# Kernel optimization log

Hardware: AMD Instinct MI355X
Metric: run time of the kernel (lower is better)

Reference implementation:

```python
import jax, jax.numpy as jnp
import numpy as np

# Production GravNet config: 8 events x 4096 hits, K=40 neighbours, 4 spatial dims
B, V, K, S, P, F_IN, F_OUT = 8, 4096, 40, 4, 64, 64, 128
N = B * V
MAX_RADIUS_SQ = 1.0  # SelectKnn(max_radius=1.0)


def setup_inputs() -> dict:
    key = jax.random.key(0)
    ks = jax.random.split(key, 7)
    x = jax.random.normal(ks[0], (N, F_IN), jnp.float32)
    # Dense layer params (glorot-ish scaling)
    W_prop = jax.random.normal(ks[1], (F_IN, P), jnp.float32) / np.sqrt(F_IN)
    b_prop = jnp.zeros((P,), jnp.float32)
    W_sp = jax.random.normal(ks[2], (F_IN, S), jnp.float32) / np.sqrt(F_IN)
    b_sp = jnp.zeros((S,), jnp.float32)
    # output transform input dim = n_prop_total (2*P) + F_IN
    W_out = jax.random.normal(ks[3], (2 * P + F_IN, F_OUT), jnp.float32) / np.sqrt(2 * P + F_IN)
    b_out = jnp.zeros((F_OUT,), jnp.float32)
    row_splits = jnp.arange(B + 1, dtype=jnp.int32) * V  # equal-size ragged segments
    return dict(x=x, W_prop=W_prop, b_prop=b_prop, W_sp=W_sp, b_sp=b_sp,
                W_out=W_out, b_out=b_out, row_splits=row_splits)


def _knn_indices(coords):
    """Per-event brute-force KNN. coords: [N,S] -> global neighbour idx [N,K]."""
    c = coords.reshape(B, V, S)
    # pairwise squared distances within each event: [B,V,V]
    d = jnp.sum((c[:, :, None, :] - c[:, None, :, :]) ** 2, axis=-1)
    neg_d, idx = jax.lax.top_k(-d, K + 1)  # nearest first; col 0 is self (d=0)
    idx, dsq = idx[:, :, 1:], -neg_d[:, :, 1:]
    # tf_compatible max_radius: out-of-radius neighbours -> self index
    self_idx = jnp.arange(V, dtype=idx.dtype)[None, :, None]
    idx = jnp.where(dsq > MAX_RADIUS_SQ, self_idx, idx)
    gidx = idx + (jnp.arange(B, dtype=idx.dtype) * V)[:, None, None]
    return gidx.reshape(N, K)


def reference(x, W_prop, b_prop, W_sp, b_sp, W_out, b_out, row_splits):
    coords = x @ W_sp + b_sp                      # [N,S] learned coordinates
    nidx = _knn_indices(coords)                   # [N,K] (int, non-diff)
    nb_coords = coords[nidx]                      # [N,K,S] gather
    dsq = jnp.sum((coords[:, None, :] - nb_coords) ** 2, axis=-1)  # [N,K]
    feat = x @ W_prop + b_prop                    # [N,P]
    w = jnp.exp(-10.0 * dsq)[:, :, None]          # gauss_of_lin(10*d^2)
    nf = feat[nidx] * w                           # [N,K,P]
    agg = jnp.concatenate([nf.max(axis=1), nf.mean(axis=1)], axis=-1)  # [N,2P]
    out = jnp.tanh(jnp.concatenate([agg, x], axis=-1) @ W_out + b_out)  # [N,F_OUT]
    return out
```

## Files before the change

kernel.cpp:

```cpp
#include <hip/hip_runtime.h>
#include <cstdint>
#include <cstddef>

#define NB   8
#define VV   4096
#define KNN  40
#define NTOT 32768
#define CAP  224
#define INFB 0x7F800000u
#define ONEB 0x3F800000u

__device__ __forceinline__ int xbucket(float x) {
  int b = (int)floorf((x + 4.f) * 32.f);
  return b < 0 ? 0 : (b > 255 ? 255 : b);
}

__global__ __launch_bounds__(256) void k_prep(
    const float* __restrict__ x, const float* __restrict__ W_prop,
    const float* __restrict__ b_prop, const float* __restrict__ W_sp,
    const float* __restrict__ b_sp, const float* __restrict__ W_out,
    float* __restrict__ coords, float* __restrict__ feat,
    float* __restrict__ xW)
{
  __shared__ float xt[64][64];
  const int t = threadIdx.x;
  const int row0 = blockIdx.x * 64;

  #pragma unroll
  for (int i = 0; i < 16; ++i) {
    int idx = t + i * 256;
    xt[idx >> 6][idx & 63] = x[(size_t)row0 * 64 + idx];
  }
  __syncthreads();

  {
    const int col = t & 63, rb = (t >> 6) * 16;
    float acc[16];
    #pragma unroll
    for (int i = 0; i < 16; ++i) acc[i] = b_prop[col];
    for (int k = 0; k < 64; k += 4) {
      const float w0 = W_prop[(k + 0) * 64 + col];
      const float w1 = W_prop[(k + 1) * 64 + col];
      const float w2 = W_prop[(k + 2) * 64 + col];
      const float w3 = W_prop[(k + 3) * 64 + col];
      #pragma unroll
      for (int i = 0; i < 16; ++i) {
        const float4 a4 = *(const float4*)&xt[rb + i][k];
        acc[i] += a4.x * w0 + a4.y * w1 + a4.z * w2 + a4.w * w3;
      }
    }
    #pragma unroll
    for (int i = 0; i < 16; ++i)
      feat[(size_t)(row0 + rb + i) * 64 + col] = acc[i];
  }

  {
    const int col = t & 127, who = t >> 7;
    #pragma unroll
    for (int p = 0; p < 2; ++p) {
      const int rb = who * 16 + p * 32;
      float acc[16];
      #pragma unroll
      for (int i = 0; i < 16; ++i) acc[i] = 0.f;
      for (int k = 0; k < 64; k += 4) {
        const float w0 = W_out[(size_t)(128 + k + 0) * 128 + col];
        const float w1 = W_out[(size_t)(128 + k + 1) * 128 + col];
        const float w2 = W_out[(size_t)(128 + k + 2) * 128 + col];
        const float w3 = W_out[(size_t)(128 + k + 3) * 128 + col];
        #pragma unroll
        for (int i = 0; i < 16; ++i) {
          const float4 a4 = *(const float4*)&xt[rb + i][k];
          acc[i] += a4.x * w0 + a4.y * w1 + a4.z * w2 + a4.w * w3;
        }
      }
      #pragma unroll
      for (int i = 0; i < 16; ++i)
        xW[(size_t)(row0 + rb + i) * 128 + col] = acc[i];
    }
  }

  if (t < 64) {
    float a0 = b_sp[0], a1 = b_sp[1], a2 = b_sp[2], a3 = b_sp[3];
    for (int k = 0; k < 64; ++k) {
      const float xv = xt[t][k];
      a0 += xv * W_sp[k * 4 + 0];
      a1 += xv * W_sp[k * 4 + 1];
      a2 += xv * W_sp[k * 4 + 2];
      a3 += xv * W_sp[k * 4 + 3];
    }
    ((float4*)coords)[row0 + t] = make_float4(a0, a1, a2, a3);
  }
}

__global__ __launch_bounds__(512) void k_sort(
    float* __restrict__ coords, unsigned short* __restrict__ perm,
    unsigned short* __restrict__ prefg)
{
  __shared__ float4 cs[VV];
  __shared__ int hist[256];
  __shared__ int pref[257];
  const int t = threadIdx.x, ev = blockIdx.x;
  const int evbase = ev * VV;
  float4* cg = (float4*)coords + evbase;

  for (int i = t; i < VV; i += 512) cs[i] = cg[i];
  if (t < 256) hist[t] = 0;
  __syncthreads();

  for (int i = t; i < VV; i += 512)
    atomicAdd(&hist[xbucket(cs[i].x)], 1);
  __syncthreads();

  if (t < 64) {
    const int l = t;
    const int h0 = hist[4*l], h1 = hist[4*l+1], h2 = hist[4*l+2], h3 = hist[4*l+3];
    const int s = h0 + h1 + h2 + h3;
    int incl = s;
    #pragma unroll
    for (int off = 1; off < 64; off <<= 1) {
      const int v = __shfl_up(incl, off);
      if (l >= off) incl += v;
    }
    const int excl = incl - s;
    pref[4*l]   = excl;
    pref[4*l+1] = excl + h0;
    pref[4*l+2] = excl + h0 + h1;
    pref[4*l+3] = excl + h0 + h1 + h2;
    if (l == 63) pref[256] = excl + s;
  }
  __syncthreads();
  if (t < 256) hist[t] = 0;
  __syncthreads();

  for (int i = t; i < VV; i += 512) {
    const int b = xbucket(cs[i].x);
    const int pos = pref[b] + atomicAdd(&hist[b], 1);
    cg[pos] = cs[i];
    perm[evbase + pos] = (unsigned short)i;
  }
  if (t < 257) prefg[ev * 257 + t] = (unsigned short)pref[t];
}

template <int NC>
__device__ __forceinline__ unsigned bs40(const uint2* __restrict__ list,
                                         int M, int lane) {
  unsigned dv[NC];
  #pragma unroll
  for (int j = 0; j < NC; ++j) {
    const int e = lane + j * 64;
    dv[j] = (e < M) ? list[e].x : INFB;
  }
  unsigned lo = 0, hi = ONEB;
  while (lo < hi) {
    const unsigned mid = (lo + hi) >> 1;
    int cnt = 0;
    #pragma unroll
    for (int j = 0; j < NC; ++j)
      cnt += (int)__popcll(__ballot(dv[j] <= mid));
    if (cnt >= KNN) hi = mid; else lo = mid + 1;
  }
  return hi;
}

#define AGG_CHUNK(J0, N)                                                     \
  {                                                                          \
    float fv[N], wgt[N];                                                     \
    _Pragma("unroll")                                                        \
    for (int j = 0; j < N; ++j) {                                            \
      const uint2 en = list[(J0) + j];                                       \
      wgt[j] = __expf(-10.f * __uint_as_float(en.x));                        \
      const int ei = __builtin_amdgcn_readfirstlane((int)en.y);              \
      fv[j] = fe[(size_t)ei * 64 + lane];                                    \
    }                                                                        \
    _Pragma("unroll")                                                        \
    for (int j = 0; j < N; ++j) {                                            \
      const float v = fv[j] * wgt[j];                                        \
      vmax = fmaxf(vmax, v);                                                 \
      vsum += v;                                                             \
    }                                                                        \
  }

__global__ __launch_bounds__(512, 4) void k_knn(
    const float* __restrict__ coords,
    const unsigned short* __restrict__ perm,
    const unsigned short* __restrict__ prefg,
    const float* __restrict__ feat, float* __restrict__ agg)
{
  __shared__ float4 cs[VV];
  __shared__ uint2 lists[8][CAP];
  __shared__ unsigned short pr[257];

  const int t = threadIdx.x, lane = t & 63;
  const int wvid = __builtin_amdgcn_readfirstlane(t) >> 6;
  const int bid0 = blockIdx.x;
  const int bid = (bid0 & 7) * 64 + (bid0 >> 3);
  const int ev = bid >> 6;
  const int slot = bid & 63;
  const int evbase = ev * VV;

  {
    const float4* cg = (const float4*)coords + evbase;
    for (int i = t; i < VV; i += 512) cs[i] = cg[i];
    if (t < 257) pr[t] = prefg[ev * 257 + t];
  }
  __syncthreads();

  uint2* list = lists[wvid];
  const float* fe = feat + (size_t)evbase * 64;
  const unsigned long long lmask = (1ull << lane) - 1ull;

  auto scan = [&](unsigned rbits, int q, float4 qc, int lo, int hi) -> int {
    int M = 0;
    #pragma unroll 4
    for (int base = lo; base < hi; base += 64) {
      const int c = base + lane;
      const float4 cc = cs[c];
      const float dx = qc.x - cc.x, dy = qc.y - cc.y;
      const float dz = qc.z - cc.z, dw = qc.w - cc.w;
      const float dsq = dx * dx + dy * dy + dz * dz + dw * dw;
      const bool pred = (__float_as_uint(dsq) <= rbits) && (c != q);
      const unsigned long long bm = __ballot(pred);
      if (pred) {
        const int pos = M + (int)__popcll(bm & lmask);
        if (pos < CAP)
          list[pos] = make_uint2(__float_as_uint(dsq), (unsigned)c);
      }
      M += (int)__popcll(bm);
    }
    return M;
  };

  for (int qi = 0; qi < 8; ++qi) {
    const int q = slot + (qi * 8 + wvid) * 64;
    const float4 qc = cs[q];
    const int origq = (int)perm[evbase + q];
    const int bq = xbucket(qc.x);
    const int wlo = ((int)pr[bq > 32 ? bq - 32 : 0]) & ~63;
    const int whi0 = (int)pr[bq + 33 > 256 ? 256 : bq + 33];
    const int whi = (whi0 + 63) & ~63;

    int M = scan(ONEB, q, qc, wlo, whi);
    bool ok = true;

    if (M > CAP) {
      const unsigned t0 = bs40<4>(list, CAP, lane);
      M = scan(t0, q, qc, wlo, whi);
      ok = (M <= CAP);
    }

    float vmax = -__builtin_inff(), vsum = 0.f;

    if (ok) {
      for (int be = 0; be < M; be += 64) {
        const int e = be + lane;
        if (e < M) {
          uint2 en = list[e];
          en.y = (unsigned)perm[evbase + (int)en.y];
          list[e] = en;
        }
      }

      int Msel;
      if (M > KNN) {
        unsigned taub;
        if      (M <=  64) taub = bs40<1>(list, M, lane);
        else if (M <= 128) taub = bs40<2>(list, M, lane);
        else               taub = bs40<4>(list, M, lane);
        int S = 0;
        for (int be = 0; be < M; be += 64) {
          const int e = be + lane;
          uint2 en = make_uint2(0u, 0u);
          bool p = false;
          if (e < M) { en = list[e]; p = (en.x <= taub); }
          const unsigned long long bm = __ballot(p);
          if (p) list[S + (int)__popcll(bm & lmask)] = en;
          S += (int)__popcll(bm);
        }
        Msel = S;
      } else {
        if (lane >= M && lane < KNN)
          list[lane] = make_uint2(0u, (unsigned)origq);
        Msel = KNN;
      }

      if (Msel == KNN) {
        AGG_CHUNK(0, 16)
        AGG_CHUNK(16, 16)
        AGG_CHUNK(32, 8)
      } else {
        #pragma unroll 4
        for (int e = 0; e < Msel; ++e) {
          const uint2 en = list[e];
          const int ei = __builtin_amdgcn_readfirstlane((int)en.y);
          const float w = __expf(-10.f * __uint_as_float(en.x));
          const float v = fe[(size_t)ei * 64 + lane] * w;
          vmax = fmaxf(vmax, v);
          vsum += v;
        }
      }
    } else {
      unsigned lo = 0, hi = ONEB;
      while (lo < hi) {
        const unsigned mid = (lo + hi) >> 1;
        const float fm = __uint_as_float(mid);
        int cnt = 0;
        for (int base = wlo; base < whi; base += 64) {
          const int c = base + lane;
          const float4 cc = cs[c];
          const float dx = qc.x - cc.x, dy = qc.y - cc.y;
          const float dz = qc.z - cc.z, dw = qc.w - cc.w;
          const float dsq = dx * dx + dy * dy + dz * dz + dw * dw;
          cnt += (int)__popcll(__ballot(dsq <= fm && c != q));
        }
        if (cnt >= KNN) hi = mid; else lo = mid + 1;
      }
      const float tau = __uint_as_float(hi);
      for (int c = wlo; c < whi; ++c) {
        if (c == q) continue;
        const float4 cc = cs[c];
        const float dx = qc.x - cc.x, dy = qc.y - cc.y;
        const float dz = qc.z - cc.z, dw = qc.w - cc.w;
        const float dsq = dx * dx + dy * dy + dz * dz + dw * dw;
        if (dsq <= tau) {
          const int ei = (int)perm[evbase + c];
          const float w = __expf(-10.f * dsq);
          const float v = fe[(size_t)ei * 64 + lane] * w;
          vmax = fmaxf(vmax, v);
          vsum += v;
        }
      }
    }

    const int g = evbase + origq;
    agg[(size_t)g * 128 + lane]      = vmax;
    agg[(size_t)g * 128 + 64 + lane] = vsum * (1.f / 40.f);
  }
}

__global__ __launch_bounds__(256) void k_out(
    const float* __restrict__ agg, const float* __restrict__ W_out,
    const float* __restrict__ b_out, float* __restrict__ out)
{
  __shared__ float at[64][128];
  const int t = threadIdx.x;
  const int row0 = blockIdx.x * 64;

  #pragma unroll
  for (int i = 0; i < 32; ++i) {
    int idx = t + i * 256;
    at[idx >> 7][idx & 127] = agg[(size_t)row0 * 128 + idx];
  }
  __syncthreads();

  const int col = t & 127, who = t >> 7;
  #pragma unroll
  for (int p = 0; p < 2; ++p) {
    const int rb = who * 16 + p * 32;
    float acc[16];
    #pragma unroll
    for (int i = 0; i < 16; ++i) acc[i] = 0.f;
    for (int k = 0; k < 128; k += 4) {
      const float w0 = W_out[(size_t)(k + 0) * 128 + col];
      const float w1 = W_out[(size_t)(k + 1) * 128 + col];
      const float w2 = W_out[(size_t)(k + 2) * 128 + col];
      const float w3 = W_out[(size_t)(k + 3) * 128 + col];
      #pragma unroll
      for (int i = 0; i < 16; ++i) {
        const float4 a4 = *(const float4*)&at[rb + i][k];
        acc[i] += a4.x * w0 + a4.y * w1 + a4.z * w2 + a4.w * w3;
      }
    }
    const float bb = b_out[col];
    #pragma unroll
    for (int i = 0; i < 16; ++i) {
      const size_t o = (size_t)(row0 + rb + i) * 128 + col;
      float v = acc[i] + bb + out[o];
      v = fminf(15.f, fmaxf(-15.f, v));
      const float e = __expf(2.f * v);
      out[o] = (e - 1.f) / (e + 1.f);
    }
  }
}

extern "C" void kernel_launch(void* const* d_in, const int* in_sizes, int n_in,
                              void* d_out, int out_size, void* d_ws, size_t ws_size,
                              hipStream_t stream) {
  const float* x      = (const float*)d_in[0];
  const float* W_prop = (const float*)d_in[1];
  const float* b_prop = (const float*)d_in[2];
  const float* W_sp   = (const float*)d_in[3];
  const float* b_sp   = (const float*)d_in[4];
  const float* W_out  = (const float*)d_in[5];
  const float* b_out  = (const float*)d_in[6];

  float* out = (float*)d_out;
  char* ws = (char*)d_ws;
  float* coords          = (float*)ws;
  float* feat            = (float*)(ws + (512 << 10));
  float* agg             = (float*)(ws + (512 << 10) + (8 << 20));
  unsigned short* perm   = (unsigned short*)(ws + (512 << 10) + (24 << 20));
  unsigned short* prefg  = (unsigned short*)(ws + (512 << 10) + (24 << 20) + (64 << 10));

  k_prep<<<NTOT / 64, 256, 0, stream>>>(x, W_prop, b_prop, W_sp, b_sp, W_out,
                                        coords, feat, out );
  k_sort<<<NB, 512, 0, stream>>>(coords, perm, prefg);
  k_knn<<<NB * (VV / 64), 512, 0, stream>>>(coords, perm, prefg, feat, agg);
  k_out<<<NTOT / 64, 256, 0, stream>>>(agg, W_out, b_out, out);
}
```

Baseline: 177.2 us.

## Split per-event bucket sort into fused global histogram and multi-block scatter

The bucket histogram moves into k_prep through global atomics, and the single-block-per-event sort kernel is replaced by a scatter kernel with 8 blocks per event that uses global cursor atomics. Sorted coords go to a separate buffer rather than being permuted in place. This spreads the serial, 8-block sort across 64 blocks to cut its latency. In exchange it adds a memset and global atomic contention, and each scatter block recomputes the prefix sum.

```diff
diff --git a/kernel.cpp b/kernel.cpp
--- a/kernel.cpp
+++ b/kernel.cpp
@@ -20,7 +20,7 @@
     const float* __restrict__ b_prop, const float* __restrict__ W_sp,
     const float* __restrict__ b_sp, const float* __restrict__ W_out,
     float* __restrict__ coords, float* __restrict__ feat,
-    float* __restrict__ xW)
+    float* __restrict__ xW, int* __restrict__ hist)
 {
   __shared__ float xt[64][64];
   const int t = threadIdx.x;
@@ -89,31 +89,26 @@
       a3 += xv * W_sp[k * 4 + 3];
     }
     ((float4*)coords)[row0 + t] = make_float4(a0, a1, a2, a3);
-  }
-}
-
-__global__ __launch_bounds__(512) void k_sort(
-    float* __restrict__ coords, unsigned short* __restrict__ perm,
-    unsigned short* __restrict__ prefg)
+    const int ev = (row0 + t) >> 12;
+    atomicAdd(&hist[ev * 256 + xbucket(a0)], 1);
+  }
+}
+
+__global__ __launch_bounds__(512) void k_scatter(
+    const float* __restrict__ coords, float* __restrict__ csort,
+    unsigned short* __restrict__ perm, const int* __restrict__ hist,
+    int* __restrict__ cursorDelta, unsigned short* __restrict__ prefg)
 {
-  __shared__ float4 cs[VV];
-  __shared__ int hist[256];
   __shared__ int pref[257];
-  const int t = threadIdx.x, ev = blockIdx.x;
+  const int t = threadIdx.x;
+  const int ev = blockIdx.x >> 3;
+  const int i = ((blockIdx.x & 7) << 9) + t;
   const int evbase = ev * VV;
-  float4* cg = (float4*)coords + evbase;
-
-  for (int i = t; i < VV; i += 512) cs[i] = cg[i];
-  if (t < 256) hist[t] = 0;
-  __syncthreads();
-
-  for (int i = t; i < VV; i += 512)
-    atomicAdd(&hist[xbucket(cs[i].x)], 1);
-  __syncthreads();
 
   if (t < 64) {
+    const int* h = hist + ev * 256;
     const int l = t;
-    const int h0 = hist[4*l], h1 = hist[4*l+1], h2 = hist[4*l+2], h3 = hist[4*l+3];
+    const int h0 = h[4*l], h1 = h[4*l+1], h2 = h[4*l+2], h3 = h[4*l+3];
     const int s = h0 + h1 + h2 + h3;
     int incl = s;
     #pragma unroll
@@ -129,16 +124,15 @@
     if (l == 63) pref[256] = excl + s;
   }
   __syncthreads();
-  if (t < 256) hist[t] = 0;
-  __syncthreads();
-
-  for (int i = t; i < VV; i += 512) {
-    const int b = xbucket(cs[i].x);
-    const int pos = pref[b] + atomicAdd(&hist[b], 1);
-    cg[pos] = cs[i];
-    perm[evbase + pos] = (unsigned short)i;
-  }
-  if (t < 257) prefg[ev * 257 + t] = (unsigned short)pref[t];
+
+  const float4 c = ((const float4*)coords)[evbase + i];
+  const int b = xbucket(c.x);
+  const int pos = pref[b] + atomicAdd(&cursorDelta[ev * 256 + b], 1);
+  ((float4*)csort)[evbase + pos] = c;
+  perm[evbase + pos] = (unsigned short)i;
+
+  if ((blockIdx.x & 7) == 0 && t < 257)
+    prefg[ev * 257 + t] = (unsigned short)pref[t];
 }
 
 template <int NC>
@@ -395,15 +389,21 @@
 
   float* out = (float*)d_out;
   char* ws = (char*)d_ws;
-  float* coords          = (float*)ws;
-  float* feat            = (float*)(ws + (512 << 10));
-  float* agg             = (float*)(ws + (512 << 10) + (8 << 20));
-  unsigned short* perm   = (unsigned short*)(ws + (512 << 10) + (24 << 20));
-  unsigned short* prefg  = (unsigned short*)(ws + (512 << 10) + (24 << 20) + (64 << 10));
-
+  float* coords          = (float*)(ws);
+  float* csort           = (float*)(ws + (512 << 10));
+  float* feat            = (float*)(ws + (1 << 20));
+  float* agg             = (float*)(ws + (9 << 20));
+  unsigned short* perm   = (unsigned short*)(ws + (25 << 20));
+  unsigned short* prefg  = (unsigned short*)(ws + (25 << 20) + 65536);
+  int* hist              = (int*)(ws + (25 << 20) + 65536 + 4608);
+  int* cursorDelta       = (int*)(ws + (25 << 20) + 65536 + 4608 + 8192);
+
+  hipMemsetAsync(hist, 0, 16384, stream);
   k_prep<<<NTOT / 64, 256, 0, stream>>>(x, W_prop, b_prop, W_sp, b_sp, W_out,
-                                        coords, feat, out );
-  k_sort<<<NB, 512, 0, stream>>>(coords, perm, prefg);
-  k_knn<<<NB * (VV / 64), 512, 0, stream>>>(coords, perm, prefg, feat, agg);
+                                        coords, feat, out ,
+                                        hist);
+  k_scatter<<<NB * 8, 512, 0, stream>>>(coords, csort, perm, hist,
+                                        cursorDelta, prefg);
+  k_knn<<<NB * (VV / 64), 512, 0, stream>>>(csort, perm, prefg, feat, agg);
   k_out<<<NTOT / 64, 256, 0, stream>>>(agg, W_out, b_out, out);
 }
```

Result: slower. 184.9 us (+4.4%).
